# Kernel optimization log

Measured on AMD Instinct MI355X. Metric: run time of the kernel, lower is better.

Reference implementation:

```python
import math
import jax, jax.numpy as jnp
import numpy as np
from jax import lax

LEAKY_SLOPE = 0.2
ACT_GAIN = math.sqrt(2.0)

def bilinear_filter():
    h = jnp.array([1.0, 3.0, 3.0, 1.0], dtype=jnp.float32)
    h = h[:, None] * h[None, :]
    return h / jnp.sum(h)

def setup_inputs() -> dict:
    key = jax.random.key(0)
    ks = jax.random.split(key, 6)
    B, Cin, Cout, W_DIM, R = 16, 512, 512, 512, 64
    return {
        "x": jax.random.normal(ks[0], (B, Cin, R // 2, R // 2), dtype=jnp.float32),
        "w": jax.random.normal(ks[1], (B, W_DIM), dtype=jnp.float32),
        "noise_raw": jax.random.normal(ks[2], (B, 1, R, R), dtype=jnp.float32),
        "affine_weight": jax.random.normal(ks[3], (Cin, W_DIM), dtype=jnp.float32),
        "affine_bias": jnp.ones((Cin,), dtype=jnp.float32),
        "weight": jax.random.normal(ks[4], (Cout, Cin, 3, 3), dtype=jnp.float32),
        "bias": 0.1 * jax.random.normal(ks[5], (Cout,), dtype=jnp.float32),
        "noise_strength": jnp.float32(1.0),
    }

def reference(x, w, noise_raw, affine_weight, affine_bias, weight, bias, noise_strength):
    B, Cin = x.shape[0], x.shape[1]
    Cout = weight.shape[0]
    w_dim = affine_weight.shape[1]
    # EqualizedLinear affine: weight_gain = 1/sqrt(in), bias_gain = 1, no activation
    styles = w @ (affine_weight * (1.0 / math.sqrt(w_dim))).T + affine_bias  # [B, Cin]
    # demodulation coefficients from modulated weights
    wmod = weight[None] * styles[:, None, :, None, None]                      # [B,Cout,Cin,3,3]
    dcoefs = lax.rsqrt(jnp.sum(jnp.square(wmod), axis=(2, 3, 4)) + 1e-8)     # [B, Cout]
    # modulate input instead of weights
    xs = x * styles[:, :, None, None]
    # up=True path: conv_transpose2d(x, weight.transpose(0,1), stride=2, padding=0)
    # == dilated conv with spatially flipped kernel, pad k-1=2
    w_flip = weight[:, :, ::-1, ::-1]
    y = lax.conv_general_dilated(
        xs, w_flip, window_strides=(1, 1), padding=[(2, 2), (2, 2)],
        lhs_dilation=(2, 2), dimension_numbers=("NCHW", "OIHW", "NCHW"))    # [B,Cout,2H+1,2H+1]
    # filter2d with 4x4 bilinear kernel, gain=4, padding=1 (depthwise)
    f = bilinear_filter() * 4.0
    kd = jnp.tile(f[None, None], (Cout, 1, 1, 1))                            # [Cout,1,4,4]
    y = lax.conv_general_dilated(
        y, kd, window_strides=(1, 1), padding=[(1, 1), (1, 1)],
        dimension_numbers=("NCHW", "OIHW", "NCHW"), feature_group_count=Cout)  # [B,Cout,2H,2H]
    # addcmul: noise + y * dcoefs
    noise = noise_raw * noise_strength
    y = noise + y * dcoefs[:, :, None, None]
    # bias, act gain sqrt(2), leaky relu 0.2
    y = (y + bias[None, :, None, None]) * ACT_GAIN
    return jnp.where(y >= 0, y, LEAKY_SLOPE * y)
```

## Files before the change

### kernel.cpp

```cpp
#include <hip/hip_runtime.h>
#include <hip/hip_bf16.h>
#include <stdint.h>

typedef float f32x4 __attribute__((ext_vector_type(4)));
typedef __bf16 bf16x8 __attribute__((ext_vector_type(8)));

#define GLDS16(gp, lp) __builtin_amdgcn_global_load_lds( \
    (const __attribute__((address_space(1))) void*)(gp), \
    (__attribute__((address_space(3))) void*)(lp), 16, 0, 0)

static __device__ __forceinline__ unsigned short f2bf(float f) {
    unsigned int u = __float_as_uint(f);
    u = (u + 0x7fffu + ((u >> 16) & 1u)) >> 16;
    return (unsigned short)u;
}
static __device__ __forceinline__ float bf2f(unsigned short v) {
    return __uint_as_float(((unsigned int)v) << 16);
}

#define O_STYLES 0
#define O_DCOEF  32768
#define O_XS     65536
#define O_WP     19005440
#define O_Y1     23724032
#define O_WSQ    23724032
#define WS_NEED  96075776
#define SP 1104

__global__ __launch_bounds__(256) void k_styles(const float* __restrict__ w,
                                                const float* __restrict__ aw,
                                                const float* __restrict__ ab,
                                                float* __restrict__ styles) {
    int g = blockIdx.x * 256 + threadIdx.x;
    int b = g >> 9, ci = g & 511;
    const float4* wr = (const float4*)(w + b * 512);
    const float4* ar = (const float4*)(aw + ci * 512);
    float acc = 0.f;
    for (int k = 0; k < 128; ++k) {
        float4 wv = wr[k], av = ar[k];
        acc += wv.x * av.x + wv.y * av.y + wv.z * av.z + wv.w * av.w;
    }
    styles[g] = acc * 0.04419417382415922f + ab[ci];
}

__global__ __launch_bounds__(256) void k_wprep(const float* __restrict__ weight,
                                               float* __restrict__ wsq,
                                               unsigned short* __restrict__ wp) {
    int g = blockIdx.x * 256 + threadIdx.x;
    const float* wb = weight + (long)g * 9;
    float v[9]; float s = 0.f;
#pragma unroll
    for (int t = 0; t < 9; ++t) { v[t] = wb[t]; s += v[t] * v[t]; }
    wsq[g] = s;
    const int wri[9] = {2, 2, 0, 0, 2, 0, 1, 1, 1};
    const int wci[9] = {2, 0, 2, 0, 1, 1, 2, 0, 1};
#pragma unroll
    for (int t = 0; t < 9; ++t)
        wp[t * 262144 + g] = f2bf(v[wri[t] * 3 + wci[t]]);
}

__global__ __launch_bounds__(256) void k_dcoef(const float* __restrict__ styles,
                                               const float* __restrict__ wsq,
                                               float* __restrict__ dcoefs) {
    int g = blockIdx.x * 256 + threadIdx.x;
    int b = g >> 9, co = g & 511;
    const float4* sr = (const float4*)(styles + b * 512);
    const float4* qr = (const float4*)(wsq + co * 512);
    float acc = 1e-8f;
    for (int k = 0; k < 128; ++k) {
        float4 sv = sr[k], qv = qr[k];
        acc += sv.x * sv.x * qv.x + sv.y * sv.y * qv.y + sv.z * sv.z * qv.z + sv.w * sv.w * qv.w;
    }
    dcoefs[g] = rsqrtf(acc);
}

__global__ __launch_bounds__(256) void k_xprep(const float* __restrict__ x,
                                               const float* __restrict__ styles,
                                               unsigned short* __restrict__ xs) {
    __shared__ float T[128][33];
    int bid = blockIdx.x;
    int cc = bid & 3, i = (bid >> 2) & 31, b = bid >> 7;
    int t = threadIdx.x;
    int ci0 = cc * 128;
    int j_r = t & 31, cl_r = t >> 5;
    const float* xp = x + (((long)(b * 512 + ci0)) * 32 + i) * 32;
#pragma unroll
    for (int it = 0; it < 16; ++it) {
        int cl = cl_r + it * 8;
        T[cl][j_r] = xp[cl * 1024 + j_r];
    }
    __syncthreads();
    int ci_w = t & 127, jg = t >> 7;
    float sv = styles[b * 512 + ci0 + ci_w];
    unsigned short* op = xs + (((long)(b * 34 + (i + 1))) * 34 + 1) * 512 + ci0 + ci_w;
#pragma unroll
    for (int jj = 0; jj < 16; ++jj) {
        int j = jg * 16 + jj;
        op[(long)j * 512] = f2bf(T[ci_w][j] * sv);
    }
}

#define BARRIER asm volatile("s_barrier" ::: "memory");
#define ST_A(kk) { GLDS16(xsB + sA0 + akt + (kk)*64, smp + nb + (kk)*16384 + t16); \
                   GLDS16(xsB + sA1 + akt + (kk)*64, smp + nb + (kk)*16384 + t16 + 8192); }
#define ST_B(kk) { GLDS16(wpB + sB0 + bkt + (kk)*64, smp + nb + 32768 + (kk)*16384 + t16); \
                   GLDS16(wpB + sB1 + bkt + (kk)*64, smp + nb + 32768 + (kk)*16384 + t16 + 8192); }
#define PHASE2(kk, STG, TAILBAR) { \
  _Pragma("unroll") for (int i = 0; i < 8; ++i) \
    av[i] = *(const bf16x8*)(smp + cb + (kk)*16384 + abase + (i*16)*64); \
  _Pragma("unroll") for (int j = 0; j < 4; ++j) \
    bv[j] = *(const bf16x8*)(smp + cb + (kk)*16384 + bbase + (j*16)*64); \
  STG; \
  asm volatile("s_waitcnt vmcnt(4)" ::: "memory"); \
  BARRIER; \
  __builtin_amdgcn_s_setprio(1); \
  _Pragma("unroll") for (int i = 0; i < 8; ++i) \
    _Pragma("unroll") for (int j = 0; j < 4; ++j) \
      acc[i][j] = __builtin_amdgcn_mfma_f32_16x16x32_bf16(av[i], bv[j], acc[i][j], 0, 0, 0); \
  __builtin_amdgcn_s_setprio(0); \
  if (TAILBAR) { BARRIER; } }

__global__ __launch_bounds__(512, 2) void k_conv(const unsigned short* __restrict__ xs,
                                                 const unsigned short* __restrict__ wp,
                                                 unsigned short* __restrict__ y1) {
    extern __shared__ __align__(16) char smem[];
    const unsigned char* xsB = (const unsigned char*)xs;
    const unsigned char* wpB = (const unsigned char*)wp;
    char* smp = smem;

    int bid = blockIdx.x;
    int par, q;
    if (bid < 138)      { par = 0; q = bid; }
    else if (bid < 276) { par = 1; q = bid - 138; }
    else if (bid < 414) { par = 2; q = bid - 276; }
    else                { par = 3; q = bid - 414; }
    int Mtile = q >> 1, Ntile = q & 1;
    int a_par = par >> 1, c_par = par & 1;
    int ntaps = a_par ? (c_par ? 1 : 2) : (c_par ? 2 : 4);
    int tapofs = (par == 0) ? 0 : ((par == 1) ? 4 : ((par == 2) ? 6 : 8));
    int NKT = ntaps << 3;

    int tid = threadIdx.x;
    int lane = tid & 63, wave = tid >> 6;
    int wm = wave >> 2, wn = wave & 3;
    int lrow = lane & 15;
    int rchunk = (((lane >> 4) ^ ((lrow >> 1) & 3)) << 4);
    int abase = (wm * 128 + lrow) * 64 + rchunk;
    int bbase = 32768 + (wn * 64 + lrow) * 64 + rchunk;

    int srow = tid >> 2;
    int schunk = (((tid & 3) ^ ((tid >> 3) & 3)) << 4);
    int sA0, sA1;
    {
        unsigned gm = (unsigned)(Mtile * 256 + srow);
        if (gm > 17471u) gm = 17471u;
        unsigned b_ = gm / 1092u; unsigned pix = gm - b_ * 1092u;
        unsigned r = pix / 33u; unsigned s = pix - r * 33u;
        sA0 = (int)(((b_ * 34u + r) * 34u + s) << 10) + schunk;
        gm = (unsigned)(Mtile * 256 + srow + 128);
        if (gm > 17471u) gm = 17471u;
        b_ = gm / 1092u; pix = gm - b_ * 1092u;
        r = pix / 33u; s = pix - r * 33u;
        sA1 = (int)(((b_ * 34u + r) * 34u + s) << 10) + schunk;
    }
    int sB0 = ((Ntile * 256 + srow) << 10) + schunk;
    int sB1 = sB0 + (128 << 10);
    int t16 = tid << 4;

    f32x4 acc[8][4];
#pragma unroll
    for (int i = 0; i < 8; ++i)
#pragma unroll
        for (int j = 0; j < 4; ++j)
            acc[i][j] = (f32x4){0.f, 0.f, 0.f, 0.f};
    bf16x8 av[8], bv[4];

    auto mkA = [&](int kt) -> int {
        int tl = kt >> 3; if (tl >= ntaps) tl = ntaps - 1;
        int cib = kt & 7;
        int dio = a_par ? 1 : (c_par ? tl : (tl >> 1));
        int djo = c_par ? 1 : (a_par ? tl : (tl & 1));
        return dio * 34816 + djo * 1024 + cib * 128;
    };
    auto mkB = [&](int kt) -> long {
        int tl = kt >> 3; if (tl >= ntaps) tl = ntaps - 1;
        return (long)(tapofs + tl) * 524288 + (long)((kt & 7) * 128);
    };

    {
        int akt = mkA(0); long bkt = mkB(0); int nb = 0;
        ST_A(0); ST_B(0); ST_A(1); ST_B(1);
    }
    asm volatile("s_waitcnt vmcnt(4)" ::: "memory");
    BARRIER;

    int cur = 0;
    for (int kt = 0; kt < NKT; ++kt) {
        int akt = mkA(kt + 1);
        long bkt = mkB(kt + 1);
        int nb = (cur ^ 1) << 16;
        int cb = cur << 16;
        PHASE2(0, { ST_A(0); ST_B(0); }, 0)
        PHASE2(1, { ST_A(1); ST_B(1); }, 1)
        cur ^= 1;
    }

#pragma unroll
    for (int mf = 0; mf < 8; ++mf) {
        int gm0 = Mtile * 256 + wm * 128 + mf * 16 + ((lane >> 4) << 2);
        if (gm0 < 17472) {
            unsigned ug = (unsigned)gm0;
            unsigned bb = ug / 1092u;
            int pix0 = (int)(ug - bb * 1092u);
            unsigned rr = (unsigned)pix0 % 33u;
            long rowb = ((long)((bb * 4u + par) * 512)) * SP;
#pragma unroll
            for (int nf = 0; nf < 4; ++nf) {
                int co = Ntile * 256 + wn * 64 + nf * 16 + lrow;
                if (pix0 <= 1084) {
                    ushort4 pk;
                    pk.x = f2bf(acc[mf][nf][0]);
                    pk.y = f2bf(acc[mf][nf][1]);
                    pk.z = f2bf(acc[mf][nf][2]);
                    pk.w = f2bf(acc[mf][nf][3]);
                    if (c_par && rr >= 29)
                        ((unsigned short*)&pk)[32 - rr] = 0;
                    *(ushort4*)(y1 + rowb + (long)co * SP + pix0) = pk;
                } else if (pix0 == 1088) {
                    y1[rowb + (long)co * SP + 1088] = c_par ? (unsigned short)0 : f2bf(acc[mf][nf][0]);
                }
            }
        }
    }
}

__global__ __launch_bounds__(256) void k_blur(const unsigned short* __restrict__ y1,
                                              const float* __restrict__ dcoefs,
                                              const float* __restrict__ bias,
                                              const float* __restrict__ noise,
                                              const float* __restrict__ nstr,
                                              float* __restrict__ out) {
    __shared__ float yl[4 * 35 * 36];
    int bid = blockIdx.x;
    int cg = bid & 127, b = bid >> 7;
    int t = threadIdx.x;
    int n = t & 63, mq = t >> 6;
    float ns = nstr[0];

    for (int i = t; i < 5040; i += 256) yl[i] = 0.f;
    __syncthreads();

    const int rvv[4] = {33, 33, 32, 32};
    const float* npb = noise + b * 4096;

    int o = n & 1;
    int se = n >> 1;
    int sp_ = se - 1 + o;
    float a0 = o ? 1.f : 3.f;
    float a1 = o ? 3.f : 1.f;

    for (int cc = 0; cc < 4; ++cc) {
        int co = cg * 4 + cc;
#pragma unroll
        for (int pl = 0; pl < 4; ++pl) {
            const unsigned short* src = y1 + ((long)((b * 4 + pl) * 512 + co)) * SP;
            float* dst = yl + pl * 1260;
            int pv = rvv[pl] * 33;
            for (int it = t; it < 273; it += 256) {
                int p0 = it * 4;
                ushort4 v = *(const ushort4*)(src + p0);
                unsigned short vv[4] = {v.x, v.y, v.z, v.w};
#pragma unroll
                for (int k = 0; k < 4; ++k) {
                    int p = p0 + k;
                    if (p < pv && p < 1089) {
                        unsigned r = (unsigned)p / 33u;
                        unsigned s = (unsigned)p - r * 33u;
                        dst[(r + 1) * 36 + (s + 1)] = bf2f(vv[k]);
                    }
                }
            }
        }
        __syncthreads();

        float dc = dcoefs[b * 512 + co];
        float bi = bias[co];
        float* ob = out + ((long)(b * 512 + co)) * 4096;

        auto H = [&](int ap, int r) -> float {
            const float* pe = yl + (ap * 2) * 1260 + (r + 1) * 36;
            const float* po = pe + 1260;
            return a0 * pe[se + 1] + a1 * pe[se + 2] + a1 * po[sp_ + 1] + a0 * po[sp_ + 2];
        };

        int m0 = mq * 16;
        int re = m0 >> 1;
        float he0 = H(0, re), he1 = H(0, re + 1);
        float ho0 = H(1, re - 1), ho1 = H(1, re);
#pragma unroll
        for (int k = 0; k < 16; k += 2) {
            int m = m0 + k;
            float ve = 3.f * he0 + he1 + ho0 + 3.f * ho1;
            float val = npb[m * 64 + n] * ns + ve * (0.0625f * dc);
            val = (val + bi) * 1.41421356237309515f;
            ob[m * 64 + n] = (val >= 0.f) ? val : 0.2f * val;
            float hn_o = H(1, re + 1);
            float vo = he0 + 3.f * he1 + 3.f * ho1 + hn_o;
            val = npb[(m + 1) * 64 + n] * ns + vo * (0.0625f * dc);
            val = (val + bi) * 1.41421356237309515f;
            ob[(m + 1) * 64 + n] = (val >= 0.f) ? val : 0.2f * val;
            ho0 = ho1; ho1 = hn_o;
            float hn_e = H(0, re + 2);
            he0 = he1; he1 = hn_e;
            re += 1;
        }
        __syncthreads();
    }
}

extern "C" void kernel_launch(void* const* d_in, const int* in_sizes, int n_in,
                              void* d_out, int out_size, void* d_ws, size_t ws_size,
                              hipStream_t stream) {
    (void)in_sizes; (void)n_in; (void)out_size;
    if (ws_size < (size_t)WS_NEED) return;
    const float* x      = (const float*)d_in[0];
    const float* w      = (const float*)d_in[1];
    const float* noise  = (const float*)d_in[2];
    const float* aw     = (const float*)d_in[3];
    const float* ab     = (const float*)d_in[4];
    const float* weight = (const float*)d_in[5];
    const float* bias   = (const float*)d_in[6];
    const float* nstr   = (const float*)d_in[7];
    float* out = (float*)d_out;
    char* ws = (char*)d_ws;
    float* styles          = (float*)(ws + O_STYLES);
    float* dcoefs          = (float*)(ws + O_DCOEF);
    unsigned short* xs     = (unsigned short*)(ws + O_XS);
    unsigned short* wp     = (unsigned short*)(ws + O_WP);
    unsigned short* y1     = (unsigned short*)(ws + O_Y1);
    float* wsq             = (float*)(ws + O_WSQ);

    hipFuncSetAttribute((const void*)k_conv,
                        hipFuncAttributeMaxDynamicSharedMemorySize, 131072);

    hipMemsetAsync(xs, 0, 18939904, stream);
    k_styles<<<32,   256, 0, stream>>>(w, aw, ab, styles);
    k_wprep <<<1024, 256, 0, stream>>>(weight, wsq, wp);
    k_dcoef <<<32,   256, 0, stream>>>(styles, wsq, dcoefs);
    k_xprep <<<2048, 256, 0, stream>>>(x, styles, xs);
    k_conv  <<<552,  512, 131072, stream>>>(xs, wp, y1);
    k_blur  <<<2048, 256, 0, stream>>>(y1, dcoefs, bias, noise, nstr, out);
}
```

Before: 221.6 us.

## Remap conv block order for L2 reuse and tighten barrier scheduling

Reorders the k_conv grid so that blocks sharing the same M tile but different N tiles are launched close together. The goal is better L2 reuse of the activation tiles across the two N halves. It also replaces the inline-asm barriers with builtin s_barrier plus sched_barrier fences and an explicit lgkmcnt wait, which constrains how the compiler orders LDS reads relative to the MFMA block. The epilogue stops zeroing boundary columns for odd-column parities and writes the raw value at pixel 1088, on the assumption that the zero-padded input already yields zeros there.

```diff
diff --git a/kernel.cpp b/kernel.cpp
--- a/kernel.cpp
+++ b/kernel.cpp
@@ -100,7 +100,6 @@
     }
 }
 
-#define BARRIER asm volatile("s_barrier" ::: "memory");
 #define ST_A(kk) { GLDS16(xsB + sA0 + akt + (kk)*64, smp + nb + (kk)*16384 + t16); \
                    GLDS16(xsB + sA1 + akt + (kk)*64, smp + nb + (kk)*16384 + t16 + 8192); }
 #define ST_B(kk) { GLDS16(wpB + sB0 + bkt + (kk)*64, smp + nb + 32768 + (kk)*16384 + t16); \
@@ -111,14 +110,17 @@
   _Pragma("unroll") for (int j = 0; j < 4; ++j) \
     bv[j] = *(const bf16x8*)(smp + cb + (kk)*16384 + bbase + (j*16)*64); \
   STG; \
+  __builtin_amdgcn_sched_barrier(0); \
   asm volatile("s_waitcnt vmcnt(4)" ::: "memory"); \
-  BARRIER; \
+  __builtin_amdgcn_s_barrier(); \
+  asm volatile("s_waitcnt lgkmcnt(0)" ::: "memory"); \
+  __builtin_amdgcn_sched_barrier(0); \
   __builtin_amdgcn_s_setprio(1); \
   _Pragma("unroll") for (int i = 0; i < 8; ++i) \
     _Pragma("unroll") for (int j = 0; j < 4; ++j) \
       acc[i][j] = __builtin_amdgcn_mfma_f32_16x16x32_bf16(av[i], bv[j], acc[i][j], 0, 0, 0); \
   __builtin_amdgcn_s_setprio(0); \
-  if (TAILBAR) { BARRIER; } }
+  if (TAILBAR) __builtin_amdgcn_s_barrier(); }
 
 __global__ __launch_bounds__(512, 2) void k_conv(const unsigned short* __restrict__ xs,
                                                  const unsigned short* __restrict__ wp,
@@ -128,13 +130,13 @@
     const unsigned char* wpB = (const unsigned char*)wp;
     char* smp = smem;
 
-    int bid = blockIdx.x;
-    int par, q;
-    if (bid < 138)      { par = 0; q = bid; }
-    else if (bid < 276) { par = 1; q = bid - 138; }
-    else if (bid < 414) { par = 2; q = bid - 276; }
-    else                { par = 3; q = bid - 414; }
-    int Mtile = q >> 1, Ntile = q & 1;
+    int d = blockIdx.x;
+    int pr, nt;
+    if (d >= 544) { int r = d - 544; pr = 272 + (r & 3); nt = r >> 2; }
+    else          { pr = (d >> 4) * 8 + (d & 7); nt = (d >> 3) & 1; }
+    int par = pr / 69;
+    int Mtile = pr - par * 69;
+    int Ntile = nt;
     int a_par = par >> 1, c_par = par & 1;
     int ntaps = a_par ? (c_par ? 1 : 2) : (c_par ? 2 : 4);
     int tapofs = (par == 0) ? 0 : ((par == 1) ? 4 : ((par == 2) ? 6 : 8));
@@ -191,8 +193,9 @@
         int akt = mkA(0); long bkt = mkB(0); int nb = 0;
         ST_A(0); ST_B(0); ST_A(1); ST_B(1);
     }
+    __builtin_amdgcn_sched_barrier(0);
     asm volatile("s_waitcnt vmcnt(4)" ::: "memory");
-    BARRIER;
+    __builtin_amdgcn_s_barrier();
 
     int cur = 0;
     for (int kt = 0; kt < NKT; ++kt) {
@@ -212,22 +215,20 @@
             unsigned ug = (unsigned)gm0;
             unsigned bb = ug / 1092u;
             int pix0 = (int)(ug - bb * 1092u);
-            unsigned rr = (unsigned)pix0 % 33u;
             long rowb = ((long)((bb * 4u + par) * 512)) * SP;
 #pragma unroll
             for (int nf = 0; nf < 4; ++nf) {
                 int co = Ntile * 256 + wn * 64 + nf * 16 + lrow;
+                unsigned short* dst = y1 + rowb + (long)co * SP + pix0;
                 if (pix0 <= 1084) {
                     ushort4 pk;
                     pk.x = f2bf(acc[mf][nf][0]);
                     pk.y = f2bf(acc[mf][nf][1]);
                     pk.z = f2bf(acc[mf][nf][2]);
                     pk.w = f2bf(acc[mf][nf][3]);
-                    if (c_par && rr >= 29)
-                        ((unsigned short*)&pk)[32 - rr] = 0;
-                    *(ushort4*)(y1 + rowb + (long)co * SP + pix0) = pk;
+                    *(ushort4*)dst = pk;
                 } else if (pix0 == 1088) {
-                    y1[rowb + (long)co * SP + 1088] = c_par ? (unsigned short)0 : f2bf(acc[mf][nf][0]);
+                    dst[0] = f2bf(acc[mf][nf][0]);
                 }
             }
         }
```

New measurement: 207.4 us. 6.4% less time.
